# Performance work log

Measured on AMD Instinct MI355X. Metric: run time of the kernel, lower is better.

Reference implementation:

```python
import jax, jax.numpy as jnp
import numpy as np

HEADS = 8
SR = 2
EPS_BN = 1e-5
EPS_LN = 1e-5


def _conv(x, w, b, stride=1, pad=0):
    y = jax.lax.conv_general_dilated(x, w, (stride, stride), [(pad, pad), (pad, pad)],
                                     dimension_numbers=('NCHW', 'OIHW', 'NCHW'))
    return y + b[None, :, None, None]


def _bn(x, g, b):
    # eval-mode BatchNorm with running_mean=0, running_var=1
    return x * (g / jnp.sqrt(1.0 + EPS_BN))[None, :, None, None] + b[None, :, None, None]


def _dwt_haar(x):
    # [B,c,H,W] -> [B,4c,H/2,W/2] stacked as LL,HL,LH,HH (Wave-ViT convention)
    x1 = x[:, :, 0::2, 0::2] / 2
    x2 = x[:, :, 1::2, 0::2] / 2
    x3 = x[:, :, 0::2, 1::2] / 2
    x4 = x[:, :, 1::2, 1::2] / 2
    ll = x1 + x2 + x3 + x4
    hl = -x1 - x2 + x3 + x4
    lh = -x1 + x2 - x3 + x4
    hh = x1 - x2 - x3 + x4
    return jnp.concatenate([ll, hl, lh, hh], axis=1)


def _idwt_haar(y):
    # [B,4c,h,w] -> [B,c,2h,2w], exact inverse of _dwt_haar
    c = y.shape[1] // 4
    ll, hl, lh, hh = y[:, :c], y[:, c:2 * c], y[:, 2 * c:3 * c], y[:, 3 * c:]
    p1 = (ll - hl - lh + hh) / 2  # (0::2, 0::2)
    p2 = (ll - hl + lh - hh) / 2  # (1::2, 0::2)
    p3 = (ll + hl - lh - hh) / 2  # (0::2, 1::2)
    p4 = (ll + hl + lh + hh) / 2  # (1::2, 1::2)
    B, _, h2, w2 = ll.shape
    row0 = jnp.stack([p1, p3], axis=-1)  # even rows
    row1 = jnp.stack([p2, p4], axis=-1)  # odd rows
    out = jnp.stack([row0, row1], axis=3)  # [B,c,h2,2,w2,2]
    return out.reshape(B, c, 2 * h2, 2 * w2)


def setup_inputs() -> dict:
    key = jax.random.key(0)
    ks = jax.random.split(key, 12)
    B, H, W, C = 8, 56, 56, 512
    N = H * W
    c4 = C // 4

    def nrm(k, shp, std):
        return jax.random.normal(k, shp, jnp.float32) * std

    return {
        'x': jax.random.normal(ks[0], (B, N, C), jnp.float32),
        'H': H, 'W': W,
        'reduce_w': nrm(ks[1], (c4, C, 1, 1), (2.0 / c4) ** 0.5),
        'reduce_b': jnp.zeros((c4,), jnp.float32),
        'reduce_g': jnp.ones((c4,), jnp.float32),
        'reduce_beta': jnp.zeros((c4,), jnp.float32),
        'filter_w': nrm(ks[2], (C, C, 3, 3), (2.0 / (9 * C)) ** 0.5),
        'filter_b': jnp.zeros((C,), jnp.float32),
        'filter_g': jnp.ones((C,), jnp.float32),
        'filter_beta': jnp.zeros((C,), jnp.float32),
        'q_w': nrm(ks[3], (C, C), 0.02),
        'q_b': jnp.zeros((C,), jnp.float32),
        'ln_g': jnp.ones((C,), jnp.float32),
        'ln_b': jnp.zeros((C,), jnp.float32),
        'kv_w': nrm(ks[4], (2 * C, C), 0.02),
        'kv_b': jnp.zeros((2 * C,), jnp.float32),
        'kve_w': nrm(ks[5], (C, C, SR, SR), (2.0 / (SR * SR * C)) ** 0.5),
        'kve_b': jnp.zeros((C,), jnp.float32),
        'proj_w': nrm(ks[6], (C, C + c4), 0.02),
        'proj_b': jnp.zeros((C,), jnp.float32),
    }


def reference(x, H, W, reduce_w, reduce_b, reduce_g, reduce_beta,
              filter_w, filter_b, filter_g, filter_beta,
              q_w, q_b, ln_g, ln_b, kv_w, kv_b, kve_w, kve_b, proj_w, proj_b):
    B, N, C = x.shape
    hd = C // HEADS
    scale = hd ** -0.5

    q = (x @ q_w.T + q_b).reshape(B, N, HEADS, hd).transpose(0, 2, 1, 3)  # [B,h,N,d]

    xi = x.reshape(B, H, W, C).transpose(0, 3, 1, 2)  # NCHW
    r = jax.nn.relu(_bn(_conv(xi, reduce_w, reduce_b), reduce_g, reduce_beta))  # [B,C/4,H,W]
    r16 = r.astype(jnp.float16)
    x_dwt = _dwt_haar(r16).astype(jnp.float32)  # [B,C,H/2,W/2]
    x_dwt = jax.nn.relu(_bn(_conv(x_dwt, filter_w, filter_b, pad=1), filter_g, filter_beta))
    x_dwt16 = x_dwt.astype(jnp.float16)
    x_idwt = _idwt_haar(x_dwt16)  # [B,C/4,H,W] fp16
    x_idwt = x_idwt.reshape(B, C // 4, H * W).transpose(0, 2, 1)  # [B,N,C/4]

    x_dwt = x_dwt16.astype(jnp.float32)
    kv_in = _conv(x_dwt, kve_w, kve_b, stride=SR).reshape(B, C, -1).transpose(0, 2, 1)  # [B,M,C]
    mu = kv_in.mean(-1, keepdims=True)
    var = ((kv_in - mu) ** 2).mean(-1, keepdims=True)
    kv_n = (kv_in - mu) / jnp.sqrt(var + EPS_LN) * ln_g + ln_b
    kv = (kv_n @ kv_w.T + kv_b).reshape(B, -1, 2, HEADS, hd).transpose(2, 0, 3, 1, 4)
    k, v = kv[0], kv[1]  # [B,h,M,d]

    attn = jax.nn.softmax(jnp.einsum('bhnd,bhmd->bhnm', q, k) * scale, axis=-1)
    o = jnp.einsum('bhnm,bhmd->bhnd', attn, v).transpose(0, 2, 1, 3).reshape(B, N, C)
    o = jnp.concatenate([o, x_idwt.astype(jnp.float32)], axis=-1)  # [B,N,C+C/4]
    return o @ proj_w.T + proj_b
```

## Files before the change

### kernel.cpp

```cpp
#include <hip/hip_runtime.h>
#include <math.h>


typedef _Float16 half8 __attribute__((ext_vector_type(8)));
typedef float f32x4 __attribute__((ext_vector_type(4)));

static const size_t OFF_X16  = 0;
static const size_t OFF_Q16  = 12845056;
static const size_t OFF_CAT  = 25690112;
static const size_t OFF_R16  = 41746432;
static const size_t OFF_PAD  = 44957696;
static const size_t OFF_DWTB = 48644096;
static const size_t OFF_QRW  = 51855360;
static const size_t OFF_LN16 = 55066624;
static const size_t OFF_KV16 = 55869440;
static const size_t OFF_WT   = 57475072;
static const size_t OFF_KT   = 59834368;
static const size_t OFF_KVW  = 61145088;
static const size_t OFF_PW   = 61669376;
static const size_t OFF_VT   = 62062592;
static const size_t OFF_PART = 62980096;

#define BN_RSQ 0.9999950000374997f
#define SCL2   0.1803368801111204f
#define PART_STRIDE 3211264
#define KVE_STRIDE  802816

__device__ __forceinline__ void async_copy16(const _Float16* g, _Float16* l) {
    __builtin_amdgcn_global_load_lds(
        (const __attribute__((address_space(1))) void*)g,
        (__attribute__((address_space(3))) void*)l, 16, 0, 0);
}

#define WAIT4_BARRIER() asm volatile("s_waitcnt vmcnt(4)\n\ts_barrier" ::: "memory")
#define WAIT2_BARRIER() asm volatile("s_waitcnt vmcnt(2)\n\ts_barrier" ::: "memory")
#define WAIT0_BARRIER() asm volatile("s_waitcnt vmcnt(0)\n\ts_barrier" ::: "memory")

template <int ALOAD, int EPI>
__global__ __launch_bounds__(256) void gemm16(
    const _Float16* __restrict__ A, const _Float16* __restrict__ W,
    void* __restrict__ outp, int M, int K, int lda, int ldc,
    const float* __restrict__ bias, void* __restrict__ outp2)
{
    __shared__ _Float16 sA[3][128 * 32];
    __shared__ _Float16 sB[3][128 * 32];
    const int t = threadIdx.x;
    const int lane = t & 63, wid = t >> 6;

    int bx = blockIdx.x, by = blockIdx.y;
    const int m0 = bx * 128, n0 = by * 128;
    const int kbase = blockIdx.z * K;

    const int sr = wid * 16 + (lane >> 2);
    const int sc = (lane & 3) * 8;
    const int stA0 = wid * 512;
    const int stA1 = 2048 + wid * 512;

    const _Float16 *aP0, *aP1;
    if constexpr (ALOAD == 0) {
        int r0 = m0 + sr;      if (r0 > M - 1) r0 = M - 1;
        int r1 = m0 + 64 + sr; if (r1 > M - 1) r1 = M - 1;
        aP0 = A + (size_t)r0 * lda + sc;
        aP1 = A + (size_t)r1 * lda + sc;
    } else {
        int m_ = m0 + sr; if (m_ > M - 1) m_ = M - 1;
        int b_ = m_ / 196, rem = m_ - b_ * 196, i_ = rem / 14, j_ = rem - i_ * 14;
        aP0 = A + ((size_t)(b_ * 784 + 2 * i_ * 28 + 2 * j_)) * 512 + sc;
        m_ = m0 + 64 + sr; if (m_ > M - 1) m_ = M - 1;
        b_ = m_ / 196; rem = m_ - b_ * 196; i_ = rem / 14; j_ = rem - i_ * 14;
        aP1 = A + ((size_t)(b_ * 784 + 2 * i_ * 28 + 2 * j_)) * 512 + sc;
    }
    const int ldw = (ALOAD == 2) ? lda : K;
    const _Float16* bP0 = W + (size_t)(n0 + sr) * ldw + sc;
    const _Float16* bP1 = W + (size_t)(n0 + 64 + sr) * ldw + sc;

    const int mw = wid & 1, nw = wid >> 1;
    const int pAoff = (mw * 64 + (lane & 15)) * 32 + (lane >> 4) * 8;
    const int pBoff = (nw * 64 + (lane & 15)) * 32 + (lane >> 4) * 8;

    f32x4 acc[4][4];
#pragma unroll
    for (int i = 0; i < 4; ++i)
#pragma unroll
        for (int j = 0; j < 4; ++j) acc[i][j] = (f32x4)(0.0f);

    auto aoff_of = [&](int k) -> int {
        if constexpr (ALOAD == 0) {
            return k;
        } else {
            int sub = k >> 9; int ky = sub >> 1, kx = sub & 1;
            return (ky * 28 + kx) * 512 + (k & 511);
        }
    };
    auto stage = [&](int ti, int buf) {
        int k = kbase + ti * 32;
        int aOff = aoff_of(k);
        async_copy16(aP0 + aOff, &sA[buf][stA0]);
        async_copy16(aP1 + aOff, &sA[buf][stA1]);
        async_copy16(bP0 + k, &sB[buf][stA0]);
        async_copy16(bP1 + k, &sB[buf][stA1]);
    };

    const int nt = K >> 5;
    stage(0, 0);
    if (nt > 1) { stage(1, 1); WAIT4_BARRIER(); }
    else        { WAIT0_BARRIER(); }

    int cur = 0;
    for (int i = 0; i < nt; ++i) {
        const _Float16* pA = &sA[cur][0] + pAoff;
        const _Float16* pB = &sB[cur][0] + pBoff;
        half8 aF[4], bF[4];
#pragma unroll
        for (int u = 0; u < 4; ++u) aF[u] = *(const half8*)(pA + u * 512);
#pragma unroll
        for (int u = 0; u < 4; ++u) bF[u] = *(const half8*)(pB + u * 512);

        const bool st = (i + 2 < nt);
        if (st) {
            int nb = cur + 2; if (nb >= 3) nb -= 3;
            stage(i + 2, nb);
        }
#pragma unroll
        for (int u = 0; u < 4; ++u)
#pragma unroll
            for (int j = 0; j < 4; ++j)
                acc[u][j] = __builtin_amdgcn_mfma_f32_16x16x32_f16(
                    aF[u], bF[j], acc[u][j], 0, 0, 0);

        if (i + 1 < nt) {
            if (st) WAIT4_BARRIER();
            else    WAIT0_BARRIER();
        }
        ++cur; if (cur == 3) cur = 0;
    }

    const int orow = m0 + mw * 64 + (lane >> 4) * 4;
    const int ocol = n0 + nw * 64 + (lane & 15);
#pragma unroll
    for (int j = 0; j < 4; ++j) {
        int col = ocol + j * 16;
        float bv = 0.0f;
        if constexpr (EPI == 5) bv = bias[col];
#pragma unroll
        for (int i = 0; i < 4; ++i) {
#pragma unroll
            for (int r = 0; r < 4; ++r) {
                int row = orow + i * 16 + r;
                if (row >= M) continue;
                float v = acc[i][j][r] + bv;
                if constexpr (EPI == 3) {
                    ((float*)outp)[(size_t)blockIdx.z * KVE_STRIDE
                                   + (size_t)row * ldc + col] = v;
                } else {
                    if (n0 >= 512) {
                        int hd_ = col - 512;
                        int h_ = hd_ >> 6, d_ = hd_ & 63;
                        int b_ = row / 196, m_ = row - b_ * 196;
                        ((_Float16*)outp2)[((size_t)((b_ * 8 + h_) * 64 + d_)) * 224
                                           + m_] = (_Float16)v;
                    } else {
                        ((_Float16*)outp)[(size_t)row * ldc + col] = (_Float16)v;
                    }
                }
            }
        }
    }
}

template <int EPI>
__global__ __launch_bounds__(512) void gemm16w8(
    const _Float16* __restrict__ A, const _Float16* __restrict__ W,
    void* __restrict__ outp, int M, int K, int lda, int ldc,
    const float* __restrict__ bias, const float* __restrict__ bng,
    const float* __restrict__ bnb, const float* __restrict__ bias2,
    void* __restrict__ outp2)
{
    __shared__ _Float16 sA[3][128 * 32];
    __shared__ _Float16 sB[3][128 * 32];
    const int t = threadIdx.x;
    const int lane = t & 63, wid = t >> 6;

    int bx = blockIdx.x, by = blockIdx.y;
    {
        int nwg = gridDim.x * gridDim.y;
        if ((nwg & 7) == 0) {
            int orig = by * gridDim.x + bx;
            int cs = nwg >> 3;
            int wg = (orig & 7) * cs + (orig >> 3);
            by = wg % gridDim.y;
            bx = wg / gridDim.y;
        }
    }
    const int m0 = bx * 128, n0 = by * 128;

    const int sr = wid * 16 + (lane >> 2);
    const int sc = (lane & 3) * 8;
    const int stO = wid * 512;

    int r0 = m0 + sr; if (r0 > M - 1) r0 = M - 1;
    const _Float16* aP = A + (size_t)r0 * lda + sc;
    const _Float16* bP = W + (size_t)(n0 + sr) * K + sc;

    const int mw = wid & 1, nw = wid >> 1;
    const int pAoff = (mw * 64 + (lane & 15)) * 32 + (lane >> 4) * 8;
    const int pBoff = (nw * 32 + (lane & 15)) * 32 + (lane >> 4) * 8;

    f32x4 acc[4][2];
#pragma unroll
    for (int i = 0; i < 4; ++i)
#pragma unroll
        for (int j = 0; j < 2; ++j) acc[i][j] = (f32x4)(0.0f);

    auto stage = [&](int ti, int buf) {
        int k = ti * 32;
        async_copy16(aP + k, &sA[buf][stO]);
        async_copy16(bP + k, &sB[buf][stO]);
    };

    const int nt = K >> 5;
    stage(0, 0);
    stage(1, 1);
    WAIT2_BARRIER();

    int cur = 0;
    for (int i = 0; i < nt; ++i) {
        const _Float16* pA = &sA[cur][0] + pAoff;
        const _Float16* pB = &sB[cur][0] + pBoff;
        half8 aF[4], bF[2];
#pragma unroll
        for (int u = 0; u < 4; ++u) aF[u] = *(const half8*)(pA + u * 512);
#pragma unroll
        for (int v = 0; v < 2; ++v) bF[v] = *(const half8*)(pB + v * 512);

        const bool st = (i + 2 < nt);
        if (st) {
            int nb = cur + 2; if (nb >= 3) nb -= 3;
            stage(i + 2, nb);
        }
#pragma unroll
        for (int u = 0; u < 4; ++u)
#pragma unroll
            for (int v = 0; v < 2; ++v)
                acc[u][v] = __builtin_amdgcn_mfma_f32_16x16x32_f16(
                    aF[u], bF[v], acc[u][v], 0, 0, 0);

        if (i + 1 < nt) {
            if (st) WAIT2_BARRIER();
            else    WAIT0_BARRIER();
        }
        ++cur; if (cur == 3) cur = 0;
    }

    const int orow = m0 + mw * 64 + (lane >> 4) * 4;
    const int ocol = n0 + nw * 32 + (lane & 15);
#pragma unroll
    for (int v = 0; v < 2; ++v) {
        int col = ocol + v * 16;
        float bv, g = 0.0f, b2 = 0.0f;
        if constexpr (EPI == 4) {
            if (n0 >= 512) {
                bv = bias2[col - 512];
                g = bng[col - 512] * BN_RSQ;
                b2 = bnb[col - 512];
            } else {
                bv = bias[col];
            }
        } else {
            bv = bias[col];
        }
#pragma unroll
        for (int u = 0; u < 4; ++u) {
#pragma unroll
            for (int r = 0; r < 4; ++r) {
                int row = orow + u * 16 + r;
                if (row >= M) continue;
                float v2 = acc[u][v][r] + bv;
                if constexpr (EPI == 0) {
                    __builtin_nontemporal_store(
                        v2, (float*)outp + (size_t)row * ldc + col);
                } else {
                    if (n0 >= 512) {
                        v2 = fmaxf(v2 * g + b2, 0.0f);
                        ((_Float16*)outp2)[(size_t)row * 128 + (col - 512)] =
                            (_Float16)v2;
                    } else {
                        ((_Float16*)outp)[(size_t)row * ldc + col] = (_Float16)v2;
                    }
                }
            }
        }
    }
}

__global__ __launch_bounds__(512) void conv_splitk(
    const _Float16* __restrict__ A, const _Float16* __restrict__ W,
    float* __restrict__ partA, float* __restrict__ partB)
{
    __shared__ _Float16 sA[3][128 * 32];
    __shared__ _Float16 sB[3][128 * 32];
    const int t = threadIdx.x;
    const int lane = t & 63, wid = t >> 6;

    int orig = blockIdx.x;
    int wg = (orig & 7) * 98 + (orig >> 3);
    int bx = wg % 49;  int c = wg / 49;
    int by = c & 3,    bz = c >> 2;

    const int m0 = bx * 128, n0 = by * 128;
    const int kbase = bz * 1152;

    const int sr = wid * 16 + (lane >> 2);
    const int sc = (lane & 3) * 8;
    const int stO = wid * 512;

    int m_ = m0 + sr;
    int b_ = m_ / 784, rem = m_ - b_ * 784, y_ = rem / 28, x_ = rem - y_ * 28;
    const _Float16* aP = A + ((size_t)(b_ * 900 + (y_ + 1) * 30 + (x_ + 1))) * 512 + sc;
    const _Float16* bP = W + (size_t)(n0 + sr) * 4608 + sc;

    const int mw = wid & 1, nw = wid >> 1;
    const int pAoff = (mw * 64 + (lane & 15)) * 32 + (lane >> 4) * 8;
    const int pBoff = (nw * 32 + (lane & 15)) * 32 + (lane >> 4) * 8;

    f32x4 acc[4][2];
#pragma unroll
    for (int i = 0; i < 4; ++i)
#pragma unroll
        for (int j = 0; j < 2; ++j) acc[i][j] = (f32x4)(0.0f);

    auto aoff_of = [&](int k) -> int {
        int sub = k >> 9; int s3 = sub / 3;
        int dy = s3 - 1, dx = sub - s3 * 3 - 1;
        return (dy * 30 + dx) * 512 + (k & 511);
    };
    auto stage = [&](int ti, int buf) {
        int k = kbase + ti * 32;
        async_copy16(aP + aoff_of(k), &sA[buf][stO]);
        async_copy16(bP + k, &sB[buf][stO]);
    };

    const int nt = 36;
    stage(0, 0);
    stage(1, 1);
    WAIT2_BARRIER();

    int cur = 0;
    for (int i = 0; i < nt; ++i) {
        const _Float16* pA = &sA[cur][0] + pAoff;
        const _Float16* pB = &sB[cur][0] + pBoff;
        half8 aF[4], bF[2];
#pragma unroll
        for (int u = 0; u < 4; ++u) aF[u] = *(const half8*)(pA + u * 512);
#pragma unroll
        for (int v = 0; v < 2; ++v) bF[v] = *(const half8*)(pB + v * 512);

        const bool st = (i + 2 < nt);
        if (st) {
            int nb = cur + 2; if (nb >= 3) nb -= 3;
            stage(i + 2, nb);
        }
#pragma unroll
        for (int u = 0; u < 4; ++u)
#pragma unroll
            for (int v = 0; v < 2; ++v)
                acc[u][v] = __builtin_amdgcn_mfma_f32_16x16x32_f16(
                    aF[u], bF[v], acc[u][v], 0, 0, 0);

        if (i + 1 < nt) {
            if (st) WAIT2_BARRIER();
            else    WAIT0_BARRIER();
        }
        ++cur; if (cur == 3) cur = 0;
    }

    float* dst = (bz < 2) ? (partA + (size_t)bz * PART_STRIDE)
                          : (partB + (size_t)(bz - 2) * PART_STRIDE);
    const int orow = m0 + mw * 64 + (lane >> 4) * 4;
    const int ocol = n0 + nw * 32 + (lane & 15);
#pragma unroll
    for (int v = 0; v < 2; ++v) {
#pragma unroll
        for (int u = 0; u < 4; ++u) {
#pragma unroll
            for (int r = 0; r < 4; ++r)
                dst[(size_t)(orow + u * 16 + r) * 512 + ocol + v * 16] = acc[u][v][r];
        }
    }
}

__global__ __launch_bounds__(128) void conv_epi_idwt(
    const float* __restrict__ pA, const float* __restrict__ pB,
    _Float16* __restrict__ dwtb, _Float16* __restrict__ cat,
    const float* __restrict__ bias, const float* __restrict__ bng,
    const float* __restrict__ bnb)
{
    int p = blockIdx.x;
    int b = p / 784; int rem = p - b * 784;
    int i = rem / 28;  int j = rem - i * 28;
    int c = threadIdx.x;
    size_t base = (size_t)p * 512;
    _Float16 g16[4];
#pragma unroll
    for (int g = 0; g < 4; ++g) {
        int ch = g * 128 + c;
        float s = (pA[base + ch] + pA[PART_STRIDE + base + ch])
                + (pB[base + ch] + pB[PART_STRIDE + base + ch]);
        float v = (s + bias[ch]) * (bng[ch] * BN_RSQ) + bnb[ch];
        g16[g] = (_Float16)fmaxf(v, 0.0f);
        dwtb[base + ch] = g16[g];
    }
    _Float16 ll = g16[0], hl = g16[1], lh = g16[2], hh = g16[3];
    _Float16 h = (_Float16)0.5f;
    _Float16 p1 = (((ll - hl) - lh) + hh) * h;
    _Float16 p2 = (((ll - hl) + lh) - hh) * h;
    _Float16 p3 = (((ll + hl) - lh) - hh) * h;
    _Float16 p4 = (((ll + hl) + lh) + hh) * h;
    int y = 2 * i, x = 2 * j;
    size_t rb = (size_t)b * 3136;
    __builtin_nontemporal_store(p1, &cat[(rb + (size_t)y * 56 + x) * 640 + 512 + c]);
    __builtin_nontemporal_store(p3, &cat[(rb + (size_t)y * 56 + x + 1) * 640 + 512 + c]);
    __builtin_nontemporal_store(p2, &cat[(rb + (size_t)(y + 1) * 56 + x) * 640 + 512 + c]);
    __builtin_nontemporal_store(p4, &cat[(rb + (size_t)(y + 1) * 56 + x + 1) * 640 + 512 + c]);
}

__device__ __forceinline__ void cvt8_at(
    const float* __restrict__ s, _Float16* __restrict__ d, int i)
{
    const float4* sp = (const float4*)(s + (size_t)i * 8);
    float4 a = sp[0], b = sp[1];
    half8 h;
    h[0] = (_Float16)a.x; h[1] = (_Float16)a.y; h[2] = (_Float16)a.z; h[3] = (_Float16)a.w;
    h[4] = (_Float16)b.x; h[5] = (_Float16)b.y; h[6] = (_Float16)b.z; h[7] = (_Float16)b.w;
    *(half8*)(d + (size_t)i * 8) = h;
}

__global__ __launch_bounds__(256) void prep_kernel(
    const float* __restrict__ qw, const float* __restrict__ rw,
    const float* __restrict__ kvw, const float* __restrict__ pw,
    const float* __restrict__ fw, const float* __restrict__ kw,
    const float* __restrict__ x,
    _Float16* __restrict__ qrw16, _Float16* __restrict__ kvw16,
    _Float16* __restrict__ pw16, _Float16* __restrict__ wT,
    _Float16* __restrict__ kT, _Float16* __restrict__ pad,
    _Float16* __restrict__ vt, _Float16* __restrict__ x16)
{
    int bid = blockIdx.x, tid = threadIdx.x;
    if (bid < 128) {
        cvt8_at(qw, qrw16, bid * 256 + tid);
    } else if (bid < 160) {
        cvt8_at(rw, qrw16 + 262144, (bid - 128) * 256 + tid);
    } else if (bid < 416) {
        cvt8_at(kvw, kvw16, (bid - 160) * 256 + tid);
    } else if (bid < 576) {
        cvt8_at(pw, pw16, (bid - 416) * 256 + tid);
    } else if (bid < 9792) {
        int idx = (bid - 576) * 256 + tid;
        int n = idx / 4608; int r = idx - n * 4608;
        int sub = r >> 9; int ci = r & 511;
        wT[idx] = (_Float16)fw[(size_t)n * 4608 + ci * 9 + sub];
    } else if (bid < 13888) {
        int idx = (bid - 9792) * 256 + tid;
        int n = idx >> 11; int r = idx & 2047;
        int sub = r >> 9; int ci = r & 511;
        kT[idx] = (_Float16)kw[((size_t)n << 11) + (ci << 2) + sub];
    } else if (bid < 15688) {
        int i = (bid - 13888) * 256 + tid;
        *(float4*)(pad + (size_t)i * 8) = make_float4(0.f, 0.f, 0.f, 0.f);
    } else if (bid < 16136) {
        int i = (bid - 15688) * 256 + tid;
        *(float4*)(vt + (size_t)i * 8) = make_float4(0.f, 0.f, 0.f, 0.f);
    } else {
        cvt8_at(x, x16, (bid - 16136) * 256 + tid);
    }
}

__global__ __launch_bounds__(128) void dwt_kernel(
    const _Float16* __restrict__ r, _Float16* __restrict__ pad)
{
    int bid = blockIdx.x;
    int b = bid / 784; int rem = bid - b * 784;
    int i = rem / 28;  int j = rem - i * 28;
    int c = threadIdx.x;
    int y = 2 * i, x = 2 * j;
    size_t base = (size_t)b * 3136;
    _Float16 f1 = r[(base + (size_t)y * 56 + x) * 128 + c];
    _Float16 f2 = r[(base + (size_t)(y + 1) * 56 + x) * 128 + c];
    _Float16 f3 = r[(base + (size_t)y * 56 + (x + 1)) * 128 + c];
    _Float16 f4 = r[(base + (size_t)(y + 1) * 56 + (x + 1)) * 128 + c];
    _Float16 h = (_Float16)0.5f;
    _Float16 x1 = f1 * h, x2 = f2 * h, x3 = f3 * h, x4 = f4 * h;
    _Float16 ll = ((x1 + x2) + x3) + x4;
    _Float16 hl = (((-x1) - x2) + x3) + x4;
    _Float16 lh = (((-x1) + x2) - x3) + x4;
    _Float16 hh = ((x1 - x2) - x3) + x4;
    size_t ob = ((size_t)b * 900 + (size_t)(i + 1) * 30 + (j + 1)) * 512;
    pad[ob + c]       = ll;
    pad[ob + 128 + c] = hl;
    pad[ob + 256 + c] = lh;
    pad[ob + 384 + c] = hh;
}

__global__ __launch_bounds__(256) void ln_kernel(
    const float* __restrict__ part, _Float16* __restrict__ o,
    const float* __restrict__ g, const float* __restrict__ bta,
    const float* __restrict__ kvb)
{
    int wave = threadIdx.x >> 6;
    int lane = threadIdx.x & 63;
    int row = blockIdx.x * 4 + wave;
    int c = lane * 8;
    const float* rp = part + (size_t)row * 512 + c;
    float v[8];
#pragma unroll
    for (int i = 0; i < 8; i += 4) {
        float4 a0 = *(const float4*)(rp + i);
        float4 a1 = *(const float4*)(rp + KVE_STRIDE + i);
        float4 a2 = *(const float4*)(rp + 2 * KVE_STRIDE + i);
        float4 a3 = *(const float4*)(rp + 3 * KVE_STRIDE + i);
        v[i + 0] = (a0.x + a1.x) + (a2.x + a3.x) + kvb[c + i + 0];
        v[i + 1] = (a0.y + a1.y) + (a2.y + a3.y) + kvb[c + i + 1];
        v[i + 2] = (a0.z + a1.z) + (a2.z + a3.z) + kvb[c + i + 2];
        v[i + 3] = (a0.w + a1.w) + (a2.w + a3.w) + kvb[c + i + 3];
    }
    float s = ((v[0] + v[1]) + (v[2] + v[3])) + ((v[4] + v[5]) + (v[6] + v[7]));
#pragma unroll
    for (int off = 32; off; off >>= 1) s += __shfl_xor(s, off);
    float mu = s * (1.0f / 512.0f);
    float sq = 0.0f;
#pragma unroll
    for (int i = 0; i < 8; ++i) { v[i] -= mu; sq += v[i] * v[i]; }
#pragma unroll
    for (int off = 32; off; off >>= 1) sq += __shfl_xor(sq, off);
    float inv = 1.0f / sqrtf(sq * (1.0f / 512.0f) + 1e-5f);
    half8 hv;
#pragma unroll
    for (int i = 0; i < 8; ++i) hv[i] = (_Float16)(v[i] * inv * g[c + i] + bta[c + i]);
    *(half8*)(o + (size_t)row * 512 + c) = hv;
}

__global__ __launch_bounds__(256) void attn_mfma(
    const _Float16* __restrict__ q, const _Float16* __restrict__ kv,
    const _Float16* __restrict__ vt, _Float16* __restrict__ cat)
{
    __shared__ _Float16 sK[64][72];
    __shared__ _Float16 sVT[64][72];
    __shared__ _Float16 sP[4][16][40];
    int bid = blockIdx.x;
    int qt = bid % 49;
    int h  = (bid / 49) & 7;
    int b  = bid / 392;
    int n0 = qt * 64;
    int t = threadIdx.x, lane = t & 63, wid = t >> 6;
    int quad = lane >> 4, l16 = lane & 15;

    const _Float16* qp = q + ((size_t)(b * 3136 + n0 + wid * 16 + l16)) * 512
                           + h * 64 + quad * 8;
    half8 aQ0 = *(const half8*)qp;
    half8 aQ1 = *(const half8*)(qp + 32);

    f32x4 oacc[4];
#pragma unroll
    for (int i = 0; i < 4; ++i) oacc[i] = (f32x4)(0.0f);
    float lsum[4] = {0.f, 0.f, 0.f, 0.f};

    const _Float16* vtb = vt + ((size_t)((b * 8 + h) * 64)) * 224;

    for (int c0 = 0; c0 < 224; c0 += 64) {
        __syncthreads();
#pragma unroll
        for (int it = 0; it < 2; ++it) {
            int slot = t + 256 * it;
            int row = slot >> 3, c8 = (slot & 7) * 8;
            int m = c0 + row; if (m > 195) m = 195;
            *(half8*)&sK[row][c8] =
                *(const half8*)(kv + ((size_t)(b * 196 + m)) * 1024 + h * 64 + c8);
        }
#pragma unroll
        for (int it = 0; it < 2; ++it) {
            int slot = t + 256 * it;
            int row = slot >> 3, c8 = (slot & 7) * 8;
            *(half8*)&sVT[row][c8] =
                *(const half8*)(vtb + (size_t)row * 224 + c0 + c8);
        }
        __syncthreads();

#pragma unroll
        for (int sc = 0; sc < 64; sc += 32) {
            half8 bk00 = *(const half8*)&sK[sc + l16][quad * 8];
            half8 bk01 = *(const half8*)&sK[sc + l16][32 + quad * 8];
            half8 bk10 = *(const half8*)&sK[sc + 16 + l16][quad * 8];
            half8 bk11 = *(const half8*)&sK[sc + 16 + l16][32 + quad * 8];
            f32x4 s0 = (f32x4)(0.0f), s1 = (f32x4)(0.0f);
            __builtin_amdgcn_s_setprio(1);
            s0 = __builtin_amdgcn_mfma_f32_16x16x32_f16(aQ0, bk00, s0, 0, 0, 0);
            s0 = __builtin_amdgcn_mfma_f32_16x16x32_f16(aQ1, bk01, s0, 0, 0, 0);
            s1 = __builtin_amdgcn_mfma_f32_16x16x32_f16(aQ0, bk10, s1, 0, 0, 0);
            s1 = __builtin_amdgcn_mfma_f32_16x16x32_f16(aQ1, bk11, s1, 0, 0, 0);
            __builtin_amdgcn_s_setprio(0);

            int col0 = c0 + sc + l16;
            float msk0 = (col0 < 196) ? 0.0f : -INFINITY;
            float msk1 = (col0 + 16 < 196) ? 0.0f : -INFINITY;
            float p0[4], p1[4];
#pragma unroll
            for (int r = 0; r < 4; ++r) {
                p0[r] = exp2f(s0[r] * SCL2 + msk0);
                p1[r] = exp2f(s1[r] * SCL2 + msk1);
                lsum[r] += p0[r] + p1[r];
            }
#pragma unroll
            for (int r = 0; r < 4; ++r) {
                sP[wid][quad * 4 + r][l16]      = (_Float16)p0[r];
                sP[wid][quad * 4 + r][16 + l16] = (_Float16)p1[r];
            }
            half8 aP = *(const half8*)&sP[wid][l16][quad * 8];
            half8 bv0 = *(const half8*)&sVT[l16][sc + quad * 8];
            half8 bv1 = *(const half8*)&sVT[16 + l16][sc + quad * 8];
            half8 bv2 = *(const half8*)&sVT[32 + l16][sc + quad * 8];
            half8 bv3 = *(const half8*)&sVT[48 + l16][sc + quad * 8];
            __builtin_amdgcn_s_setprio(1);
            oacc[0] = __builtin_amdgcn_mfma_f32_16x16x32_f16(aP, bv0, oacc[0], 0, 0, 0);
            oacc[1] = __builtin_amdgcn_mfma_f32_16x16x32_f16(aP, bv1, oacc[1], 0, 0, 0);
            oacc[2] = __builtin_amdgcn_mfma_f32_16x16x32_f16(aP, bv2, oacc[2], 0, 0, 0);
            oacc[3] = __builtin_amdgcn_mfma_f32_16x16x32_f16(aP, bv3, oacc[3], 0, 0, 0);
            __builtin_amdgcn_s_setprio(0);
        }
    }

    float inv[4];
#pragma unroll
    for (int r = 0; r < 4; ++r) {
        float s = lsum[r];
        s += __shfl_xor(s, 1);
        s += __shfl_xor(s, 2);
        s += __shfl_xor(s, 4);
        s += __shfl_xor(s, 8);
        inv[r] = 1.0f / s;
    }
#pragma unroll
    for (int r = 0; r < 4; ++r) {
        size_t rowoff = ((size_t)(b * 3136 + n0 + wid * 16 + quad * 4 + r)) * 640
                        + h * 64 + l16;
#pragma unroll
        for (int tv = 0; tv < 4; ++tv)
            cat[rowoff + tv * 16] = (_Float16)(oacc[tv][r] * inv[r]);
    }
}

extern "C" void kernel_launch(void* const* d_in, const int* in_sizes, int n_in,
                              void* d_out, int out_size, void* d_ws, size_t ws_size,
                              hipStream_t stream)
{
    const float* x           = (const float*)d_in[0];
    const float* reduce_w    = (const float*)d_in[3];
    const float* reduce_b    = (const float*)d_in[4];
    const float* reduce_g    = (const float*)d_in[5];
    const float* reduce_beta = (const float*)d_in[6];
    const float* filter_w    = (const float*)d_in[7];
    const float* filter_b    = (const float*)d_in[8];
    const float* filter_g    = (const float*)d_in[9];
    const float* filter_beta = (const float*)d_in[10];
    const float* q_w         = (const float*)d_in[11];
    const float* q_b         = (const float*)d_in[12];
    const float* ln_g        = (const float*)d_in[13];
    const float* ln_b        = (const float*)d_in[14];
    const float* kv_w        = (const float*)d_in[15];
    const float* kv_b        = (const float*)d_in[16];
    const float* kve_w       = (const float*)d_in[17];
    const float* kve_b       = (const float*)d_in[18];
    const float* proj_w      = (const float*)d_in[19];
    const float* proj_b      = (const float*)d_in[20];
    float* out = (float*)d_out;
    _Float16* hws = (_Float16*)d_ws;

    _Float16* x16    = hws + OFF_X16;
    _Float16* q16    = hws + OFF_Q16;
    _Float16* cat16  = hws + OFF_CAT;
    _Float16* r16    = hws + OFF_R16;
    _Float16* pad16  = hws + OFF_PAD;
    _Float16* dwtb16 = hws + OFF_DWTB;
    _Float16* qrw16  = hws + OFF_QRW;
    _Float16* ln16   = hws + OFF_LN16;
    _Float16* kv16   = hws + OFF_KV16;
    _Float16* wT16   = hws + OFF_WT;
    _Float16* kT16   = hws + OFF_KT;
    _Float16* kvw16  = hws + OFF_KVW;
    _Float16* pw16   = hws + OFF_PW;
    _Float16* vt16   = hws + OFF_VT;
    float*    partA  = (float*)(hws + OFF_X16);
    float*    partB  = (float*)(hws + OFF_PART);
    float*    kvepart = (float*)(hws + OFF_X16);

    prep_kernel<<<dim3(22408), dim3(256), 0, stream>>>(
        q_w, reduce_w, kv_w, proj_w, filter_w, kve_w, x,
        qrw16, kvw16, pw16, wT16, kT16, pad16, vt16, x16);

    gemm16w8<4><<<dim3(196, 5), dim3(512), 0, stream>>>(
        x16, qrw16, q16, 25088, 512, 512, 512, q_b, reduce_g, reduce_beta,
        reduce_b, r16);

    dwt_kernel<<<dim3(6272), dim3(128), 0, stream>>>(r16, pad16);

    conv_splitk<<<dim3(784), dim3(512), 0, stream>>>(pad16, wT16, partA, partB);

    conv_epi_idwt<<<dim3(6272), dim3(128), 0, stream>>>(
        partA, partB, dwtb16, cat16, filter_b, filter_g, filter_beta);

    gemm16<2, 3><<<dim3(13, 4, 4), dim3(256), 0, stream>>>(
        dwtb16, kT16, kvepart, 1568, 512, 2048, 512, nullptr, nullptr);

    ln_kernel<<<dim3(392), dim3(256), 0, stream>>>(kvepart, ln16, ln_g, ln_b, kve_b);

    gemm16<0, 5><<<dim3(13, 8), dim3(256), 0, stream>>>(
        ln16, kvw16, kv16, 1568, 512, 512, 1024, kv_b, vt16);

    attn_mfma<<<dim3(3136), dim3(256), 0, stream>>>(q16, kv16, vt16, cat16);

    gemm16w8<0><<<dim3(196, 4), dim3(512), 0, stream>>>(
        cat16, pw16, out, 25088, 640, 640, 512, proj_b, nullptr, nullptr,
        nullptr, nullptr);
}
```

Measured before the change: 380.9 us.

## Enlarge GEMM and conv tiles to 256x128 with 64x64 per-wave subtiles

The 8-wave GEMM kernels (QR projection, output projection) and the split-K conv kernel now compute 256x128 output tiles instead of 128x128. Each wave owns a 64x64 subtile with a 4x4 MFMA accumulator grid, and each k-step issues two A async loads per thread, with the wait counts adjusted to match. This raises MFMA work per LDS fragment read and per global load and halves the grid size, cutting redundant B-tile traffic. In exchange it uses more registers and LDS, lowers the number of workgroups (400 for the conv), and the conv needs row clamping and masked stores for the partial last tile.

```diff
diff --git a/kernel.cpp b/kernel.cpp
--- a/kernel.cpp
+++ b/kernel.cpp
@@ -33,7 +33,7 @@
 }
 
 #define WAIT4_BARRIER() asm volatile("s_waitcnt vmcnt(4)\n\ts_barrier" ::: "memory")
-#define WAIT2_BARRIER() asm volatile("s_waitcnt vmcnt(2)\n\ts_barrier" ::: "memory")
+#define WAIT3_BARRIER() asm volatile("s_waitcnt vmcnt(3)\n\ts_barrier" ::: "memory")
 #define WAIT0_BARRIER() asm volatile("s_waitcnt vmcnt(0)\n\ts_barrier" ::: "memory")
 
 template <int ALOAD, int EPI>
@@ -169,14 +169,14 @@
 }
 
 template <int EPI>
-__global__ __launch_bounds__(512) void gemm16w8(
+__global__ __launch_bounds__(512, 4) void gemm256(
     const _Float16* __restrict__ A, const _Float16* __restrict__ W,
     void* __restrict__ outp, int M, int K, int lda, int ldc,
     const float* __restrict__ bias, const float* __restrict__ bng,
     const float* __restrict__ bnb, const float* __restrict__ bias2,
     void* __restrict__ outp2)
 {
-    __shared__ _Float16 sA[3][128 * 32];
+    __shared__ _Float16 sA[3][256 * 32];
     __shared__ _Float16 sB[3][128 * 32];
     const int t = threadIdx.x;
     const int lane = t & 63, wid = t >> 6;
@@ -192,46 +192,49 @@
             bx = wg / gridDim.y;
         }
     }
-    const int m0 = bx * 128, n0 = by * 128;
+    const int m0 = bx * 256, n0 = by * 128;
 
     const int sr = wid * 16 + (lane >> 2);
     const int sc = (lane & 3) * 8;
     const int stO = wid * 512;
 
-    int r0 = m0 + sr; if (r0 > M - 1) r0 = M - 1;
-    const _Float16* aP = A + (size_t)r0 * lda + sc;
+    int r0 = m0 + sr;       if (r0 > M - 1) r0 = M - 1;
+    int r1 = m0 + 128 + sr; if (r1 > M - 1) r1 = M - 1;
+    const _Float16* aP0 = A + (size_t)r0 * lda + sc;
+    const _Float16* aP1 = A + (size_t)r1 * lda + sc;
     const _Float16* bP = W + (size_t)(n0 + sr) * K + sc;
 
-    const int mw = wid & 1, nw = wid >> 1;
+    const int mw = wid & 3, nw = wid >> 2;
     const int pAoff = (mw * 64 + (lane & 15)) * 32 + (lane >> 4) * 8;
-    const int pBoff = (nw * 32 + (lane & 15)) * 32 + (lane >> 4) * 8;
-
-    f32x4 acc[4][2];
-#pragma unroll
-    for (int i = 0; i < 4; ++i)
-#pragma unroll
-        for (int j = 0; j < 2; ++j) acc[i][j] = (f32x4)(0.0f);
+    const int pBoff = (nw * 64 + (lane & 15)) * 32 + (lane >> 4) * 8;
+
+    f32x4 acc[4][4];
+#pragma unroll
+    for (int u = 0; u < 4; ++u)
+#pragma unroll
+        for (int v = 0; v < 4; ++v) acc[u][v] = (f32x4)(0.0f);
 
     auto stage = [&](int ti, int buf) {
         int k = ti * 32;
-        async_copy16(aP + k, &sA[buf][stO]);
+        async_copy16(aP0 + k, &sA[buf][stO]);
+        async_copy16(aP1 + k, &sA[buf][4096 + stO]);
         async_copy16(bP + k, &sB[buf][stO]);
     };
 
     const int nt = K >> 5;
     stage(0, 0);
     stage(1, 1);
-    WAIT2_BARRIER();
+    WAIT3_BARRIER();
 
     int cur = 0;
     for (int i = 0; i < nt; ++i) {
         const _Float16* pA = &sA[cur][0] + pAoff;
         const _Float16* pB = &sB[cur][0] + pBoff;
-        half8 aF[4], bF[2];
+        half8 aF[4], bF[4];
 #pragma unroll
         for (int u = 0; u < 4; ++u) aF[u] = *(const half8*)(pA + u * 512);
 #pragma unroll
-        for (int v = 0; v < 2; ++v) bF[v] = *(const half8*)(pB + v * 512);
+        for (int v = 0; v < 4; ++v) bF[v] = *(const half8*)(pB + v * 512);
 
         const bool st = (i + 2 < nt);
         if (st) {
@@ -241,21 +244,21 @@
 #pragma unroll
         for (int u = 0; u < 4; ++u)
 #pragma unroll
-            for (int v = 0; v < 2; ++v)
+            for (int v = 0; v < 4; ++v)
                 acc[u][v] = __builtin_amdgcn_mfma_f32_16x16x32_f16(
                     aF[u], bF[v], acc[u][v], 0, 0, 0);
 
         if (i + 1 < nt) {
-            if (st) WAIT2_BARRIER();
+            if (st) WAIT3_BARRIER();
             else    WAIT0_BARRIER();
         }
         ++cur; if (cur == 3) cur = 0;
     }
 
     const int orow = m0 + mw * 64 + (lane >> 4) * 4;
-    const int ocol = n0 + nw * 32 + (lane & 15);
-#pragma unroll
-    for (int v = 0; v < 2; ++v) {
+    const int ocol = n0 + nw * 64 + (lane & 15);
+#pragma unroll
+    for (int v = 0; v < 4; ++v) {
         int col = ocol + v * 16;
         float bv, g = 0.0f, b2 = 0.0f;
         if constexpr (EPI == 4) {
@@ -293,41 +296,44 @@
     }
 }
 
-__global__ __launch_bounds__(512) void conv_splitk(
+__global__ __launch_bounds__(512, 4) void conv_splitk(
     const _Float16* __restrict__ A, const _Float16* __restrict__ W,
     float* __restrict__ partA, float* __restrict__ partB)
 {
-    __shared__ _Float16 sA[3][128 * 32];
+    __shared__ _Float16 sA[3][256 * 32];
     __shared__ _Float16 sB[3][128 * 32];
     const int t = threadIdx.x;
     const int lane = t & 63, wid = t >> 6;
 
     int orig = blockIdx.x;
-    int wg = (orig & 7) * 98 + (orig >> 3);
-    int bx = wg % 49;  int c = wg / 49;
+    int wg = (orig & 7) * 50 + (orig >> 3);
+    int bx = wg % 25;  int c = wg / 25;
     int by = c & 3,    bz = c >> 2;
 
-    const int m0 = bx * 128, n0 = by * 128;
+    const int m0 = bx * 256, n0 = by * 128;
     const int kbase = bz * 1152;
 
     const int sr = wid * 16 + (lane >> 2);
     const int sc = (lane & 3) * 8;
     const int stO = wid * 512;
 
-    int m_ = m0 + sr;
+    int m_ = m0 + sr; if (m_ > 6271) m_ = 6271;
     int b_ = m_ / 784, rem = m_ - b_ * 784, y_ = rem / 28, x_ = rem - y_ * 28;
-    const _Float16* aP = A + ((size_t)(b_ * 900 + (y_ + 1) * 30 + (x_ + 1))) * 512 + sc;
+    const _Float16* aP0 = A + ((size_t)(b_ * 900 + (y_ + 1) * 30 + (x_ + 1))) * 512 + sc;
+    m_ = m0 + 128 + sr; if (m_ > 6271) m_ = 6271;
+    b_ = m_ / 784; rem = m_ - b_ * 784; y_ = rem / 28; x_ = rem - y_ * 28;
+    const _Float16* aP1 = A + ((size_t)(b_ * 900 + (y_ + 1) * 30 + (x_ + 1))) * 512 + sc;
     const _Float16* bP = W + (size_t)(n0 + sr) * 4608 + sc;
 
-    const int mw = wid & 1, nw = wid >> 1;
+    const int mw = wid & 3, nw = wid >> 2;
     const int pAoff = (mw * 64 + (lane & 15)) * 32 + (lane >> 4) * 8;
-    const int pBoff = (nw * 32 + (lane & 15)) * 32 + (lane >> 4) * 8;
-
-    f32x4 acc[4][2];
-#pragma unroll
-    for (int i = 0; i < 4; ++i)
-#pragma unroll
-        for (int j = 0; j < 2; ++j) acc[i][j] = (f32x4)(0.0f);
+    const int pBoff = (nw * 64 + (lane & 15)) * 32 + (lane >> 4) * 8;
+
+    f32x4 acc[4][4];
+#pragma unroll
+    for (int u = 0; u < 4; ++u)
+#pragma unroll
+        for (int v = 0; v < 4; ++v) acc[u][v] = (f32x4)(0.0f);
 
     auto aoff_of = [&](int k) -> int {
         int sub = k >> 9; int s3 = sub / 3;
@@ -336,24 +342,26 @@
     };
     auto stage = [&](int ti, int buf) {
         int k = kbase + ti * 32;
-        async_copy16(aP + aoff_of(k), &sA[buf][stO]);
+        int aOff = aoff_of(k);
+        async_copy16(aP0 + aOff, &sA[buf][stO]);
+        async_copy16(aP1 + aOff, &sA[buf][4096 + stO]);
         async_copy16(bP + k, &sB[buf][stO]);
     };
 
     const int nt = 36;
     stage(0, 0);
     stage(1, 1);
-    WAIT2_BARRIER();
+    WAIT3_BARRIER();
 
     int cur = 0;
     for (int i = 0; i < nt; ++i) {
         const _Float16* pA = &sA[cur][0] + pAoff;
         const _Float16* pB = &sB[cur][0] + pBoff;
-        half8 aF[4], bF[2];
+        half8 aF[4], bF[4];
 #pragma unroll
         for (int u = 0; u < 4; ++u) aF[u] = *(const half8*)(pA + u * 512);
 #pragma unroll
-        for (int v = 0; v < 2; ++v) bF[v] = *(const half8*)(pB + v * 512);
+        for (int v = 0; v < 4; ++v) bF[v] = *(const half8*)(pB + v * 512);
 
         const bool st = (i + 2 < nt);
         if (st) {
@@ -363,12 +371,12 @@
 #pragma unroll
         for (int u = 0; u < 4; ++u)
 #pragma unroll
-            for (int v = 0; v < 2; ++v)
+            for (int v = 0; v < 4; ++v)
                 acc[u][v] = __builtin_amdgcn_mfma_f32_16x16x32_f16(
                     aF[u], bF[v], acc[u][v], 0, 0, 0);
 
         if (i + 1 < nt) {
-            if (st) WAIT2_BARRIER();
+            if (st) WAIT3_BARRIER();
             else    WAIT0_BARRIER();
         }
         ++cur; if (cur == 3) cur = 0;
@@ -377,14 +385,17 @@
     float* dst = (bz < 2) ? (partA + (size_t)bz * PART_STRIDE)
                           : (partB + (size_t)(bz - 2) * PART_STRIDE);
     const int orow = m0 + mw * 64 + (lane >> 4) * 4;
-    const int ocol = n0 + nw * 32 + (lane & 15);
-#pragma unroll
-    for (int v = 0; v < 2; ++v) {
+    const int ocol = n0 + nw * 64 + (lane & 15);
+#pragma unroll
+    for (int v = 0; v < 4; ++v) {
 #pragma unroll
         for (int u = 0; u < 4; ++u) {
 #pragma unroll
-            for (int r = 0; r < 4; ++r)
-                dst[(size_t)(orow + u * 16 + r) * 512 + ocol + v * 16] = acc[u][v][r];
+            for (int r = 0; r < 4; ++r) {
+                int row = orow + u * 16 + r;
+                if (row < 6272)
+                    dst[(size_t)row * 512 + ocol + v * 16] = acc[u][v][r];
+            }
         }
     }
 }
@@ -696,13 +707,13 @@
         q_w, reduce_w, kv_w, proj_w, filter_w, kve_w, x,
         qrw16, kvw16, pw16, wT16, kT16, pad16, vt16, x16);
 
-    gemm16w8<4><<<dim3(196, 5), dim3(512), 0, stream>>>(
+    gemm256<4><<<dim3(98, 5), dim3(512), 0, stream>>>(
         x16, qrw16, q16, 25088, 512, 512, 512, q_b, reduce_g, reduce_beta,
         reduce_b, r16);
 
     dwt_kernel<<<dim3(6272), dim3(128), 0, stream>>>(r16, pad16);
 
-    conv_splitk<<<dim3(784), dim3(512), 0, stream>>>(pad16, wT16, partA, partB);
+    conv_splitk<<<dim3(400), dim3(512), 0, stream>>>(pad16, wT16, partA, partB);
 
     conv_epi_idwt<<<dim3(6272), dim3(128), 0, stream>>>(
         partA, partB, dwtb16, cat16, filter_b, filter_g, filter_beta);
@@ -717,7 +728,7 @@
 
     attn_mfma<<<dim3(3136), dim3(256), 0, stream>>>(q16, kv16, vt16, cat16);
 
-    gemm16w8<0><<<dim3(196, 4), dim3(512), 0, stream>>>(
+    gemm256<0><<<dim3(98, 4), dim3(512), 0, stream>>>(
         cat16, pw16, out, 25088, 640, 640, 512, proj_b, nullptr, nullptr,
         nullptr, nullptr);
 }
```

Result: faster. 361.3 us (-5.2%).
